# Optimization experiments

Hardware: AMD Instinct MI355X
Metric: run time of the kernel (lower is better)

Reference implementation:

```python
import jax, jax.numpy as jnp
import numpy as np

B, C, M, K, V, D, H, A, L, HF = 2, 128, 4, 4, 64, 1024, 16, 64, 4, 2048
E = M + K
EPS = 1e-5
THETA = 10000.0


def _rmsnorm(x, w):
    return x * jax.lax.rsqrt(jnp.mean(x * x, -1, keepdims=True) + EPS) * w


def _l2norm(x):
    n = jnp.sqrt(jnp.sum(x * x, -1, keepdims=True))
    return x / jnp.maximum(n, EPS)


def _rope(x, cos, sin):
    x1, x2 = jnp.split(x, 2, axis=-1)
    return jnp.concatenate([x1 * cos + x2 * sin, -x1 * sin + x2 * cos], -1)


def _forward(x_input, dec_w1, dec_w2, pos_emb, Wqkv, Wo, Wup, Wdown, attn_norm_w, ffn_norm_w, doc):
    b = x_input.shape[0]
    c = x_input.shape[1] // M
    # decoder_w1 then 'b (c m) (k v) -> b c k (m v)', decoder_w2, pos emb
    x = jnp.einsum('bsd,od->bso', x_input, dec_w1)
    x = x.reshape(b, c, M, K, V).transpose(0, 1, 3, 2, 4).reshape(b, c, K, M * V)
    x = jnp.einsum('bcku,du->bckd', x, dec_w2) + pos_emb
    # decoder_include_original_token: prepend original m tokens per block
    x = jnp.concatenate([x_input.reshape(b, c, M, D), x], axis=2).reshape(b, c * E, D)
    s = c * E
    # mask_mod (decoder_global_original_attn): (causal & kv%e<k & same_doc) | same_block
    idx = jnp.arange(s)
    blk = idx // E
    docs = doc[:, blk]  # [b, s]
    doc_m = docs[:, :, None] == docs[:, None, :]
    causal = blk[:, None] >= blk[None, :]
    kv_ok = (idx % E) < K
    same = blk[:, None] == blk[None, :]
    mask = (causal[None] & kv_ok[None, None, :] & doc_m) | same[None]  # [b, s, s]
    # rotary tables (applied post head-split, dim A)
    inv_freq = (1.0 / THETA) ** (jnp.arange(0, A, 2) / A)
    freqs = jnp.arange(s)[:, None] * inv_freq[None, :]
    cos, sin = jnp.cos(freqs), jnp.sin(freqs)  # [s, A/2]
    scale = 1.0 / jnp.sqrt(jnp.float32(A))
    neg = jnp.float32(-1e30)

    def heads(t):
        return t.reshape(b, s, H, A).transpose(0, 2, 1, 3)

    for li in range(L):
        xn = _rmsnorm(x, attn_norm_w[li])
        qkv = jnp.einsum('bsd,od->bso', xn, Wqkv[li])
        q, k, v = jnp.split(qkv, 3, axis=-1)
        q, k, v = heads(q), heads(k), heads(v)
        q, k = _l2norm(q), _l2norm(k)  # qk_norm
        q, k = _rope(q, cos, sin), _rope(k, cos, sin)
        scores = jnp.einsum('bhqa,bhka->bhqk', q, k) * scale
        scores = jnp.where(mask[:, None], scores, neg)
        probs = jax.nn.softmax(scores, axis=-1)
        attn = jnp.einsum('bhqk,bhka->bhqa', probs, v)
        attn = attn.transpose(0, 2, 1, 3).reshape(b, s, D)
        x1_in = jnp.einsum('bsd,od->bso', attn, Wo[li]) + x
        xf = _rmsnorm(x1_in, ffn_norm_w[li])
        up = jnp.einsum('bsd,od->bso', xf, Wup[li])
        u1, u2 = jnp.split(up, 2, axis=-1)
        x = jnp.einsum('bsh,dh->bsd', jax.nn.silu(u1) * u2, Wdown[li]) + x1_in
    # 'b (c e) d -> (b c) e d' then drop original tokens
    return x.reshape(b * c, E, D)[:, M:]


def setup_inputs() -> dict:
    key = jax.random.key(0)
    ks = jax.random.split(key, 10)
    sc = 0.02
    return {
        'x_input': jax.random.normal(ks[0], (B, C * M, D), jnp.float32),
        'doc': jnp.sort(jax.random.randint(ks[1], (B, C), 0, 4), axis=-1),
        'dec_w1': jax.random.normal(ks[2], (K * V, D), jnp.float32) * sc,
        'dec_w2': jax.random.normal(ks[3], (D, M * V), jnp.float32) * sc,
        'pos_emb': jax.random.normal(ks[4], (1, 1, K, D), jnp.float32) * sc,
        'Wqkv': jax.random.normal(ks[5], (L, 3 * D, D), jnp.float32) * sc,
        'Wo': jax.random.normal(ks[6], (L, D, D), jnp.float32) * sc,
        'Wup': jax.random.normal(ks[7], (L, 2 * HF, D), jnp.float32) * sc,
        'Wdown': jax.random.normal(ks[8], (L, D, HF), jnp.float32) * sc,
        'attn_norm_w': jnp.ones((L, D), jnp.float32),
        'ffn_norm_w': jnp.ones((L, D), jnp.float32),
    }


def reference(x_input, doc, dec_w1, dec_w2, pos_emb, Wqkv, Wo, Wup, Wdown, attn_norm_w, ffn_norm_w):
    return _forward(x_input, dec_w1, dec_w2, pos_emb, Wqkv, Wo, Wup, Wdown, attn_norm_w, ffn_norm_w, doc)
```

## Files before the change

kernel.cpp:

```cpp
#include <hip/hip_runtime.h>
#include <hip/hip_bf16.h>

typedef __bf16 bf16;
typedef __bf16 bf16x8 __attribute__((ext_vector_type(8)));
typedef __bf16 bf16x4 __attribute__((ext_vector_type(4)));
typedef float  f32x4  __attribute__((ext_vector_type(4)));

#define MFMA16(a, b, c) __builtin_amdgcn_mfma_f32_16x16x32_bf16(a, b, c, 0, 0, 0)

template <int EPI, int AF32, int BF32, int TM, int TN, int SK = 1>
__global__ __launch_bounds__(256 * SK) void gemm_bt(
    const void* __restrict__ Av, const void* __restrict__ Bv,
    const float* __restrict__ Res, void* __restrict__ Out,
    int Ntot, int Ktot, int lda)
{
    constexpr int PA = TM / 64, PB = TN / 64;
    constexpr int WN = (TN == 128) ? ((TM == 128) ? 2 : 4) : 2;
    constexpr int WM = 4 / WN;
    constexpr int I = TM / (WM * 16), J = TN / (WN * 16);
    __shared__ __align__(16) bf16 As[2][SK][TM][40];
    __shared__ __align__(16) bf16 Bs[2][SK][TN][40];
    static_assert(SK == 1 || sizeof(As) >= TM * TN * 4, "combine buffer fits in As");
    const int tid  = threadIdx.x;
    const int grp  = (SK > 1) ? (tid >> 8) : 0;
    const int t8   = tid & 255;
    const int wave = t8 >> 6, lane = tid & 63;
    const int quad = lane >> 4, l16 = lane & 15;
    const int wm = wave / WN, wn = wave % WN;
    const int rowW = wm * (TM / WM), colW = wn * (TN / WN);
    const int rowBase = blockIdx.y * TM, colBase = blockIdx.x * TN;

    f32x4 acc[I][J];
    const f32x4 z4 = {0.f, 0.f, 0.f, 0.f};
#pragma unroll
    for (int i = 0; i < I; i++)
#pragma unroll
        for (int j = 0; j < J; j++) acc[i][j] = z4;

    float4 rAf[PA][2]; bf16x8 rAb[PA];
    float4 rBf[PB][2]; bf16x8 rBb[PB];

    auto loadTile = [&](int kt) {
#pragma unroll
        for (int p = 0; p < PA; p++) {
            int ch = p * 256 + t8, r = ch >> 2, c8 = (ch & 3) << 3;
            if (AF32) {
                const float* s = (const float*)Av + (size_t)(rowBase + r) * lda + kt + c8;
                rAf[p][0] = *(const float4*)s; rAf[p][1] = *(const float4*)(s + 4);
            } else {
                rAb[p] = *(const bf16x8*)((const bf16*)Av + (size_t)(rowBase + r) * lda + kt + c8);
            }
        }
#pragma unroll
        for (int p = 0; p < PB; p++) {
            int ch = p * 256 + t8, r = ch >> 2, c8 = (ch & 3) << 3;
            if (BF32) {
                const float* s = (const float*)Bv + (size_t)(colBase + r) * Ktot + kt + c8;
                rBf[p][0] = *(const float4*)s; rBf[p][1] = *(const float4*)(s + 4);
            } else {
                rBb[p] = *(const bf16x8*)((const bf16*)Bv + (size_t)(colBase + r) * Ktot + kt + c8);
            }
        }
    };
    auto storeTile = [&](int buf) {
#pragma unroll
        for (int p = 0; p < PA; p++) {
            int ch = p * 256 + t8, r = ch >> 2, c8 = (ch & 3) << 3;
            bf16x8 t;
            if (AF32) {
                t[0]=(bf16)rAf[p][0].x; t[1]=(bf16)rAf[p][0].y; t[2]=(bf16)rAf[p][0].z; t[3]=(bf16)rAf[p][0].w;
                t[4]=(bf16)rAf[p][1].x; t[5]=(bf16)rAf[p][1].y; t[6]=(bf16)rAf[p][1].z; t[7]=(bf16)rAf[p][1].w;
            } else t = rAb[p];
            *(bf16x8*)&As[buf][grp][r][c8] = t;
        }
#pragma unroll
        for (int p = 0; p < PB; p++) {
            int ch = p * 256 + t8, r = ch >> 2, c8 = (ch & 3) << 3;
            bf16x8 t;
            if (BF32) {
                t[0]=(bf16)rBf[p][0].x; t[1]=(bf16)rBf[p][0].y; t[2]=(bf16)rBf[p][0].z; t[3]=(bf16)rBf[p][0].w;
                t[4]=(bf16)rBf[p][1].x; t[5]=(bf16)rBf[p][1].y; t[6]=(bf16)rBf[p][1].z; t[7]=(bf16)rBf[p][1].w;
            } else t = rBb[p];
            *(bf16x8*)&Bs[buf][grp][r][c8] = t;
        }
    };

    const int Kgrp  = Ktot / SK;
    const int kbase = grp * Kgrp;
    loadTile(kbase);
    storeTile(0);
    __syncthreads();
    const int nk = Kgrp >> 5;
    for (int k = 0; k < nk; k++) {
        const bool more = (k + 1) < nk;
        if (more) loadTile(kbase + ((k + 1) << 5));
        const int buf = k & 1;
        bf16x8 af[I], bfr[J];
#pragma unroll
        for (int i = 0; i < I; i++)
            af[i] = *(const bf16x8*)&As[buf][grp][rowW + i * 16 + l16][quad * 8];
#pragma unroll
        for (int j = 0; j < J; j++)
            bfr[j] = *(const bf16x8*)&Bs[buf][grp][colW + j * 16 + l16][quad * 8];
#pragma unroll
        for (int i = 0; i < I; i++)
#pragma unroll
            for (int j = 0; j < J; j++)
                acc[i][j] = MFMA16(af[i], bfr[j], acc[i][j]);
        if (more) { storeTile(buf ^ 1); __syncthreads(); }
    }

    if (SK == 2) {
        __syncthreads();
        float* red = (float*)&As[0][0][0][0];
        if (grp == 1) {
#pragma unroll
            for (int i = 0; i < I; i++)
#pragma unroll
                for (int j = 0; j < J; j++)
#pragma unroll
                    for (int r = 0; r < 4; r++)
                        red[(rowW + i * 16 + quad * 4 + r) * TN +
                            (colW + j * 16 + l16)] = acc[i][j][r];
        }
        __syncthreads();
        if (grp != 0) return;
#pragma unroll
        for (int i = 0; i < I; i++)
#pragma unroll
            for (int j = 0; j < J; j++)
#pragma unroll
                for (int r = 0; r < 4; r++)
                    acc[i][j][r] += red[(rowW + i * 16 + quad * 4 + r) * TN +
                                        (colW + j * 16 + l16)];
    }

#pragma unroll
    for (int i = 0; i < I; i++) {
        int row0 = rowBase + rowW + i * 16 + quad * 4;
#pragma unroll
        for (int j = 0; j < J; j++) {
            int col = colBase + colW + j * 16 + l16;
#pragma unroll
            for (int r = 0; r < 4; r++) {
                size_t off = (size_t)(row0 + r) * Ntot + col;
                float v = acc[i][j][r];
                if (EPI == 0)      ((bf16*)Out)[off]  = (bf16)v;
                else if (EPI == 1) ((float*)Out)[off] = v + Res[off];
                else               ((float*)Out)[off] = v;
            }
        }
    }
}

__global__ __launch_bounds__(512) void gemm_up_swiglu(
    const bf16* __restrict__ A, const float* __restrict__ B,
    bf16* __restrict__ Out)
{
    __shared__ __align__(16) bf16 Smem[2][2][256][40];
    const int tid  = threadIdx.x;
    const int grp  = tid >> 8, t8 = tid & 255;
    const int wave = t8 >> 6, lane = tid & 63;
    const int quad = lane >> 4, l16 = lane & 15;
    const int wm = wave >> 1, wn = wave & 1;
    const int rowBase = blockIdx.y * 128, cb = blockIdx.x;

    f32x4 acc[4][4];
    const f32x4 z4 = {0.f, 0.f, 0.f, 0.f};
#pragma unroll
    for (int i = 0; i < 4; i++)
#pragma unroll
        for (int j = 0; j < 4; j++) acc[i][j] = z4;

    bf16x8 rA[2]; float4 rB[2][2];
    auto loadTile = [&](int kt) {
#pragma unroll
        for (int p = 0; p < 2; p++) {
            int ch = p * 256 + t8, r = ch >> 2, c8 = (ch & 3) << 3;
            rA[p] = *(const bf16x8*)(A + (size_t)(rowBase + r) * 1024 + kt + c8);
            int brow = (r >> 6) * 2048 + cb * 64 + (r & 63);
            const float* s = B + (size_t)brow * 1024 + kt + c8;
            rB[p][0] = *(const float4*)s; rB[p][1] = *(const float4*)(s + 4);
        }
    };
    auto storeTile = [&](int buf) {
#pragma unroll
        for (int p = 0; p < 2; p++) {
            int ch = p * 256 + t8, r = ch >> 2, c8 = (ch & 3) << 3;
            *(bf16x8*)&Smem[buf][grp][r][c8] = rA[p];
            bf16x8 t;
            t[0]=(bf16)rB[p][0].x; t[1]=(bf16)rB[p][0].y; t[2]=(bf16)rB[p][0].z; t[3]=(bf16)rB[p][0].w;
            t[4]=(bf16)rB[p][1].x; t[5]=(bf16)rB[p][1].y; t[6]=(bf16)rB[p][1].z; t[7]=(bf16)rB[p][1].w;
            *(bf16x8*)&Smem[buf][grp][128 + r][c8] = t;
        }
    };

    const int kbase = grp * 512;
    loadTile(kbase);
    storeTile(0);
    __syncthreads();
    for (int k = 0; k < 16; k++) {
        const bool more = k < 15;
        if (more) loadTile(kbase + ((k + 1) << 5));
        const int buf = k & 1;
        bf16x8 af[4], bfr[4];
#pragma unroll
        for (int i = 0; i < 4; i++)
            af[i] = *(const bf16x8*)&Smem[buf][grp][wm * 64 + i * 16 + l16][quad * 8];
#pragma unroll
        for (int j = 0; j < 4; j++) {
            int brow = (j < 2) ? (wn * 32 + j * 16) : (64 + wn * 32 + (j - 2) * 16);
            bfr[j] = *(const bf16x8*)&Smem[buf][grp][128 + brow + l16][quad * 8];
        }
#pragma unroll
        for (int i = 0; i < 4; i++)
#pragma unroll
            for (int j = 0; j < 4; j++)
                acc[i][j] = MFMA16(af[i], bfr[j], acc[i][j]);
        if (more) { storeTile(buf ^ 1); __syncthreads(); }
    }

    __syncthreads();
    float* red = (float*)&Smem[0][0][0][0];
    if (grp == 1) {
#pragma unroll
        for (int i = 0; i < 4; i++)
#pragma unroll
            for (int j = 0; j < 4; j++) {
                int brow = ((j < 2) ? (wn * 32 + j * 16)
                                    : (64 + wn * 32 + (j - 2) * 16)) + l16;
#pragma unroll
                for (int r = 0; r < 4; r++)
                    red[(wm * 64 + i * 16 + quad * 4 + r) * 128 + brow] = acc[i][j][r];
            }
    }
    __syncthreads();
    if (grp != 0) return;
#pragma unroll
    for (int i = 0; i < 4; i++)
#pragma unroll
        for (int j = 0; j < 4; j++) {
            int brow = ((j < 2) ? (wn * 32 + j * 16)
                                : (64 + wn * 32 + (j - 2) * 16)) + l16;
#pragma unroll
            for (int r = 0; r < 4; r++)
                acc[i][j][r] += red[(wm * 64 + i * 16 + quad * 4 + r) * 128 + brow];
        }

#pragma unroll
    for (int i = 0; i < 4; i++) {
        int row0 = rowBase + wm * 64 + i * 16 + quad * 4;
#pragma unroll
        for (int jj = 0; jj < 2; jj++) {
            int col = cb * 64 + wn * 32 + jj * 16 + l16;
#pragma unroll
            for (int r = 0; r < 4; r++) {
                float u1 = acc[i][jj][r], u2 = acc[i][jj + 2][r];
                float g = u1 / (1.f + __expf(-u1));
                Out[(size_t)(row0 + r) * 2048 + col] = (bf16)(g * u2);
            }
        }
    }
}

__global__ __launch_bounds__(256) void rmsnorm_k(
    const float* __restrict__ X, const float* __restrict__ W,
    bf16* __restrict__ Out)
{
    const int row = blockIdx.x, tid = threadIdx.x;
    const float4 xv = *(const float4*)(X + (size_t)row * 1024 + tid * 4);
    float ss = xv.x * xv.x + xv.y * xv.y + xv.z * xv.z + xv.w * xv.w;
#pragma unroll
    for (int m = 1; m < 64; m <<= 1) ss += __shfl_xor(ss, m);
    __shared__ float red[4];
    if ((tid & 63) == 0) red[tid >> 6] = ss;
    __syncthreads();
    float tot = red[0] + red[1] + red[2] + red[3];
    float sc = rsqrtf(tot * (1.0f / 1024.0f) + 1e-5f);
    const float4 wv = *(const float4*)(W + tid * 4);
    bf16x4 o;
    o[0] = (bf16)(xv.x * sc * wv.x);
    o[1] = (bf16)(xv.y * sc * wv.y);
    o[2] = (bf16)(xv.z * sc * wv.z);
    o[3] = (bf16)(xv.w * sc * wv.w);
    *(bf16x4*)(Out + (size_t)row * 1024 + tid * 4) = o;
}

__global__ __launch_bounds__(256) void ropetab_k(float* __restrict__ tab)
{
    int i = blockIdx.x * 256 + threadIdx.x;
    int s = i >> 5, j = i & 31;
    float f = (float)s * __expf(-(float)j * 0.2878231366242557f);
    tab[i * 2]     = cosf(f);
    tab[i * 2 + 1] = sinf(f);
}

__global__ __launch_bounds__(256) void qkprep_k(
    bf16* __restrict__ qkv, const float* __restrict__ tab)
{
    int wid  = blockIdx.x * 4 + (threadIdx.x >> 6);
    int lane = threadIdx.x & 63;
    int s = wid & 1023, h = (wid >> 10) & 15, b = (wid >> 14) & 1, op = wid >> 15;
    bf16* addr = qkv + ((size_t)(b * 1024 + s)) * 3072 + op * 1024 + h * 64 + lane;
    float v = (float)*addr;
    float ss = v * v;
#pragma unroll
    for (int m = 1; m < 64; m <<= 1) ss += __shfl_xor(ss, m);
    v /= fmaxf(sqrtf(ss), 1e-5f);
    float2 cssn = ((const float2*)tab)[(s << 5) + (lane & 31)];
    float partner = __shfl_xor(v, 32);
    float o = (lane < 32) ? (v * cssn.x + partner * cssn.y)
                          : (v * cssn.x - partner * cssn.y);
    if (op == 0) o *= 0.125f;
    *addr = (bf16)o;
}

__global__ __launch_bounds__(256) void vtrans_k(
    const bf16* __restrict__ qkv, bf16* __restrict__ Vt,
    float* __restrict__ Oacc, float* __restrict__ lacc)
{
    __shared__ __align__(16) bf16 Ls[64][72];
    const int st = blockIdx.x, h = blockIdx.y, b = blockIdx.z;
    const int tid = threadIdx.x;

    int gi = ((b * 16 + h) * 16 + st) * 256 + tid;
    float* Oz = Oacc + (size_t)gi * 16;
    const float4 zf = {0.f, 0.f, 0.f, 0.f};
    *(float4*)Oz = zf; *(float4*)(Oz + 4) = zf;
    *(float4*)(Oz + 8) = zf; *(float4*)(Oz + 12) = zf;
    if (gi < 32768) lacc[gi] = 0.f;

#pragma unroll
    for (int p = 0; p < 2; p++) {
        int s = p * 32 + (tid >> 3), a0 = (tid & 7) << 3;
        *(bf16x8*)&Ls[s][a0] = *(const bf16x8*)(
            qkv + ((size_t)(b * 1024 + st * 64 + s)) * 3072 + 2048 + h * 64 + a0);
    }
    __syncthreads();
#pragma unroll
    for (int p = 0; p < 2; p++) {
        int a = p * 32 + (tid >> 3), s0 = (tid & 7) << 3;
        bf16x8 v;
#pragma unroll
        for (int j = 0; j < 8; j++) v[j] = Ls[s0 + j][a];
        *(bf16x8*)(Vt + (((size_t)((b * 16 + h) * 64 + a)) << 10) + st * 64 + s0) = v;
    }
}

__global__ __launch_bounds__(256) void attn_part(
    const bf16* __restrict__ qkv, const bf16* __restrict__ Vt,
    const int* __restrict__ doc,
    float* __restrict__ Oacc, float* __restrict__ lacc)
{
    const int h = blockIdx.y, b = blockIdx.z;
    const int tid = threadIdx.x, w = tid >> 6, lane = tid & 63;
    const int quad = lane >> 4, l16 = lane & 15;

    __shared__ __align__(16) char smraw[47616];
    bf16 (*Ks)[64][72]  = (bf16(*)[64][72])(smraw);
    bf16 (*Vs)[64][72]  = (bf16(*)[64][72])(smraw + 18432);
    bf16 (*PsT)[64][20] = (bf16(*)[64][20])(smraw + 36864);
    int* docL           = (int*)(smraw + 47104);

    if (tid < 128) docL[tid] = doc[b * 128 + tid];

    int xr = blockIdx.x, p = 0, c = 0;
    for (;;) {
        int ch = (p >> 2) + 1;
        if (xr < ch) { c = xr; break; }
        xr -= ch; p++;
    }
    const int ck0 = c * 4;
    const int T   = p + 1;
    const int ck1 = (ck0 + 4 < T) ? (ck0 + 4) : T;

    const int g = 4 * p + w;
    const bf16* qp = qkv + ((size_t)(b * 1024 + g * 16 + l16)) * 3072 + h * 64 + quad * 8;
    const bf16x8 qf0 = *(const bf16x8*)qp;
    const bf16x8 qf1 = *(const bf16x8*)(qp + 32);
    const bf16* Kbase = qkv + ((size_t)(b * 1024)) * 3072 + 1024 + h * 64;
    const bf16* Vbase = Vt + (((size_t)((b * 16 + h) * 64)) << 10);

    const f32x4 z4 = {0.f, 0.f, 0.f, 0.f};
    f32x4 O[4] = {z4, z4, z4, z4};
    float lp[4] = {0.f, 0.f, 0.f, 0.f};

    __syncthreads();
    int bq[4], dq[4];
#pragma unroll
    for (int r = 0; r < 4; r++) {
        bq[r] = (g * 16 + quad * 4 + r) >> 3;
        dq[r] = docL[bq[r]];
    }

    bf16x8 rK[2], rV[2];
    auto stageRegs = [&](int kt) {
#pragma unroll
        for (int cc = 0; cc < 2; cc++) {
            int ch = cc * 256 + tid, r = ch >> 3, c8 = (ch & 7) << 3;
            rK[cc] = *(const bf16x8*)(Kbase + (size_t)(kt * 64 + r) * 3072 + c8);
            rV[cc] = *(const bf16x8*)(Vbase + ((size_t)r << 10) + kt * 64 + c8);
        }
    };
    auto stageLDS = [&](int buf) {
#pragma unroll
        for (int cc = 0; cc < 2; cc++) {
            int ch = cc * 256 + tid, r = ch >> 3, c8 = (ch & 7) << 3;
            *(bf16x8*)&Ks[buf][r][c8] = rK[cc];
            *(bf16x8*)&Vs[buf][r][c8] = rV[cc];
        }
    };

    stageRegs(ck0);
    stageLDS(0);
    __syncthreads();
    for (int kt = ck0; kt < ck1; kt++) {
        const bool more = (kt + 1) < ck1;
        if (more) stageRegs(kt + 1);
        const int buf = (kt - ck0) & 1;
        const int k0 = kt * 64;
        f32x4 sf[4];
#pragma unroll
        for (int kg = 0; kg < 4; kg++) {
            const bf16x8 k0f = *(const bf16x8*)&Ks[buf][kg * 16 + l16][quad * 8];
            const bf16x8 k1f = *(const bf16x8*)&Ks[buf][kg * 16 + l16][32 + quad * 8];
            sf[kg] = z4;
            sf[kg] = MFMA16(qf0, k0f, sf[kg]);
            sf[kg] = MFMA16(qf1, k1f, sf[kg]);
        }
        float pvv[4][4];
#pragma unroll
        for (int kg = 0; kg < 4; kg++) {
            int kgi = k0 + kg * 16 + l16;
            int bk  = kgi >> 3;
            int dkv = docL[bk];
            bool kbit = (kgi & 7) < 4;
#pragma unroll
            for (int r = 0; r < 4; r++) {
                bool ok = (bq[r] == bk) || ((bq[r] >= bk) && kbit && (dq[r] == dkv));
                float pp = ok ? __expf(sf[kg][r]) : 0.f;
                pvv[kg][r] = pp;
                lp[r] += pp;
            }
        }
#pragma unroll
        for (int kg = 0; kg < 4; kg++) {
            bf16x4 t4;
#pragma unroll
            for (int r = 0; r < 4; r++) t4[r] = (bf16)pvv[kg][r];
            *(bf16x4*)&PsT[w][kg * 16 + l16][quad * 4] = t4;
        }
        bf16x8 pa0, pa1;
#pragma unroll
        for (int j = 0; j < 8; j++) {
            pa0[j] = PsT[w][quad * 8 + j][l16];
            pa1[j] = PsT[w][32 + quad * 8 + j][l16];
        }
#pragma unroll
        for (int t = 0; t < 4; t++) {
            const bf16x8 v0f = *(const bf16x8*)&Vs[buf][t * 16 + l16][quad * 8];
            const bf16x8 v1f = *(const bf16x8*)&Vs[buf][t * 16 + l16][32 + quad * 8];
            O[t] = MFMA16(pa0, v0f, O[t]);
            O[t] = MFMA16(pa1, v1f, O[t]);
        }
        if (more) stageLDS(buf ^ 1);
        __syncthreads();
    }

    float* Osc = (float*)smraw + w * 1024;
#pragma unroll
    for (int t = 0; t < 4; t++)
#pragma unroll
        for (int r = 0; r < 4; r++)
            Osc[(quad * 4 + r) * 64 + t * 16 + l16] = O[t][r];

#pragma unroll
    for (int r = 0; r < 4; r++) {
#pragma unroll
        for (int m = 1; m < 16; m <<= 1) lp[r] += __shfl_xor(lp[r], m);
    }
    const size_t rowb = (size_t)(b * 1024 + g * 16);
    if (l16 < 4) {
        float myl = (l16 == 0) ? lp[0] : (l16 == 1) ? lp[1] : (l16 == 2) ? lp[2] : lp[3];
        atomicAdd(&lacc[(rowb + quad * 4 + l16) * 16 + h], myl);
    }

    float* Obase = Oacc + rowb * 1024 + h * 64;
#pragma unroll
    for (int i = 0; i < 16; i++)
        atomicAdd(&Obase[(size_t)i * 1024 + lane], Osc[i * 64 + lane]);
}

__global__ __launch_bounds__(256) void attn_norm(
    const float* __restrict__ Oacc, const float* __restrict__ lacc,
    bf16* __restrict__ attnb)
{
    int i8 = (blockIdx.x * 256 + threadIdx.x) * 8;
    int row = i8 >> 10, d0 = i8 & 1023;
    float inv = 1.0f / fmaxf(lacc[row * 16 + (d0 >> 6)], 1e-20f);
    const float4 a = *(const float4*)(Oacc + i8);
    const float4 bvv = *(const float4*)(Oacc + i8 + 4);
    bf16x8 o;
    o[0] = (bf16)(a.x * inv); o[1] = (bf16)(a.y * inv);
    o[2] = (bf16)(a.z * inv); o[3] = (bf16)(a.w * inv);
    o[4] = (bf16)(bvv.x * inv); o[5] = (bf16)(bvv.y * inv);
    o[6] = (bf16)(bvv.z * inv); o[7] = (bf16)(bvv.w * inv);
    *(bf16x8*)(attnb + i8) = o;
}

__global__ __launch_bounds__(256) void permute_k(
    const bf16* __restrict__ t1, bf16* __restrict__ t1p)
{
    int idx = blockIdx.x * 256 + threadIdx.x;
    int u = idx & 255, m = u >> 6, v = u & 63;
    int orow = idx >> 8;
    int k = orow & 3, bc = orow >> 2;
    int b = bc >> 7, c = bc & 127;
    t1p[idx] = t1[((size_t)(b * 512 + c * 4 + m)) * 256 + k * 64 + v];
}

__global__ __launch_bounds__(256) void buildx_k(
    const float* __restrict__ x_input, const float* __restrict__ t2,
    const float* __restrict__ pos_emb, float* __restrict__ xres)
{
    int idx = blockIdx.x * 256 + threadIdx.x;
    int d = idx & 1023, row = idx >> 10;
    int b = row >> 10, rr = row & 1023;
    int c = rr >> 3, e = rr & 7;
    float v;
    if (e < 4)
        v = x_input[((size_t)(b * 512 + c * 4 + e)) * 1024 + d];
    else
        v = t2[((size_t)(b * 512 + c * 4 + (e - 4))) * 1024 + d] +
            pos_emb[(e - 4) * 1024 + d];
    xres[idx] = v;
}

__global__ __launch_bounds__(256) void finalout_k(
    const float* __restrict__ xres, float* __restrict__ out)
{
    int idx = blockIdx.x * 256 + threadIdx.x;
    int d = idx & 1023, t = idx >> 10;
    int kk = t & 3, bc = t >> 2;
    int b = bc >> 7, c = bc & 127;
    out[idx] = xres[((size_t)(b * 1024 + c * 8 + 4 + kk)) * 1024 + d];
}

extern "C" void kernel_launch(void* const* d_in, const int* in_sizes, int n_in,
                              void* d_out, int out_size, void* d_ws, size_t ws_size,
                              hipStream_t stream)
{
    const float* x_input = (const float*)d_in[0];
    const int*   doc     = (const int*)d_in[1];
    const float* dec_w1  = (const float*)d_in[2];
    const float* dec_w2  = (const float*)d_in[3];
    const float* pos_emb = (const float*)d_in[4];
    const float* Wqkv    = (const float*)d_in[5];
    const float* Wo      = (const float*)d_in[6];
    const float* Wup     = (const float*)d_in[7];
    const float* Wdown   = (const float*)d_in[8];
    const float* anw     = (const float*)d_in[9];
    const float* fnw     = (const float*)d_in[10];
    float* out = (float*)d_out;

    char* w = (char*)d_ws;
    float* xres  = (float*)(w);
    bf16*  xn1   = (bf16*)(w + (8u << 20));
    bf16*  xn2   = (bf16*)(w + (8u << 20));
    float* Oacc  = (float*)(w + (8u << 20));
    bf16*  t1    = (bf16*)(w + (8u << 20));
    bf16*  t1p   = (bf16*)(w + (8u << 20) + (512u << 10));
    bf16*  qkv   = (bf16*)(w + (16u << 20));
    float* t2    = (float*)(w + (16u << 20));
    float* x1res = (float*)(w + (16u << 20));
    bf16*  attnb = (bf16*)(w + (24u << 20));
    bf16*  hg    = (bf16*)(w + (24u << 20));
    bf16*  Vt    = (bf16*)(w + (28u << 20));
    float* rtab  = out;
    float* lacc  = out + 131072;

    ropetab_k<<<128, 256, 0, stream>>>(rtab);
    gemm_bt<0, 1, 1, 64, 64><<<dim3(4, 16), 256, 0, stream>>>(
        x_input, dec_w1, nullptr, t1, 256, 1024, 1024);
    permute_k<<<1024, 256, 0, stream>>>(t1, t1p);
    gemm_bt<2, 0, 1, 64, 64><<<dim3(16, 16), 256, 0, stream>>>(
        t1p, dec_w2, nullptr, t2, 1024, 256, 256);
    buildx_k<<<8192, 256, 0, stream>>>(x_input, t2, pos_emb, xres);

    for (int li = 0; li < 4; ++li) {
        rmsnorm_k<<<2048, 256, 0, stream>>>(xres, anw + li * 1024, xn1);
        gemm_bt<0, 0, 1, 128, 128><<<dim3(24, 16), 256, 0, stream>>>(
            xn1, Wqkv + (size_t)li * 3072 * 1024, nullptr, qkv, 3072, 1024, 1024);
        qkprep_k<<<16384, 256, 0, stream>>>(qkv, rtab);
        vtrans_k<<<dim3(16, 16, 2), 256, 0, stream>>>(qkv, Vt, Oacc, lacc);
        attn_part<<<dim3(40, 16, 2), 256, 0, stream>>>(qkv, Vt, doc, Oacc, lacc);
        attn_norm<<<1024, 256, 0, stream>>>(Oacc, lacc, attnb);
        gemm_bt<1, 0, 1, 64, 64, 2><<<dim3(16, 32), 512, 0, stream>>>(
            attnb, Wo + (size_t)li * 1024 * 1024, xres, x1res, 1024, 1024, 1024);
        rmsnorm_k<<<2048, 256, 0, stream>>>(x1res, fnw + li * 1024, xn2);
        gemm_up_swiglu<<<dim3(32, 16), 512, 0, stream>>>(
            xn2, Wup + (size_t)li * 4096 * 1024, hg);
        gemm_bt<1, 0, 1, 64, 64, 2><<<dim3(16, 32), 512, 0, stream>>>(
            hg, Wdown + (size_t)li * 1024 * 2048, x1res, xres, 1024, 2048, 2048);
    }

    finalout_k<<<4096, 256, 0, stream>>>(xres, out);
}
```

Baseline: 898.8 us.

## Fuse attention normalization into Wo GEMM, merge prep kernels, retile QKV and up GEMMs

The attention-normalization kernel is removed. The Wo GEMM now reads the fp32 Oacc directly and scales each row-head chunk by 1/l during the bf16 conversion. The qk-prep and V-transpose kernels are merged into one launch. The QKV GEMM moves from 128x128 tiles to 64x64 tiles with a split-K of 2, which gives more blocks. The SwiGLU up GEMM drops its split-K reduction and runs the full K loop with 256 threads. Residuals are updated in place in xres and the workspace layout is reshuffled, which saves launches and memory traffic but doubles A-load bandwidth for the Wo GEMM and risks aliasing bugs.

After: 914.1 us. About the same (+1.7%).

```diff
diff --git a/kernel.cpp b/kernel.cpp
--- a/kernel.cpp
+++ b/kernel.cpp
@@ -11,8 +11,8 @@
 template <int EPI, int AF32, int BF32, int TM, int TN, int SK = 1>
 __global__ __launch_bounds__(256 * SK) void gemm_bt(
     const void* __restrict__ Av, const void* __restrict__ Bv,
-    const float* __restrict__ Res, void* __restrict__ Out,
-    int Ntot, int Ktot, int lda)
+    const float* Res, void* Out,
+    int Ntot, int Ktot, int lda, const float* __restrict__ Lsc = nullptr)
 {
     constexpr int PA = TM / 64, PB = TN / 64;
     constexpr int WN = (TN == 128) ? ((TM == 128) ? 2 : 4) : 2;
@@ -37,7 +37,7 @@
 #pragma unroll
         for (int j = 0; j < J; j++) acc[i][j] = z4;
 
-    float4 rAf[PA][2]; bf16x8 rAb[PA];
+    float4 rAf[PA][2]; bf16x8 rAb[PA]; float linv[PA];
     float4 rBf[PB][2]; bf16x8 rBb[PB];
 
     auto loadTile = [&](int kt) {
@@ -47,6 +47,8 @@
             if (AF32) {
                 const float* s = (const float*)Av + (size_t)(rowBase + r) * lda + kt + c8;
                 rAf[p][0] = *(const float4*)s; rAf[p][1] = *(const float4*)(s + 4);
+                if (AF32 == 2)
+                    linv[p] = Lsc[(size_t)(rowBase + r) * 16 + (kt >> 6)];
             } else {
                 rAb[p] = *(const bf16x8*)((const bf16*)Av + (size_t)(rowBase + r) * lda + kt + c8);
             }
@@ -68,8 +70,11 @@
             int ch = p * 256 + t8, r = ch >> 2, c8 = (ch & 3) << 3;
             bf16x8 t;
             if (AF32) {
-                t[0]=(bf16)rAf[p][0].x; t[1]=(bf16)rAf[p][0].y; t[2]=(bf16)rAf[p][0].z; t[3]=(bf16)rAf[p][0].w;
-                t[4]=(bf16)rAf[p][1].x; t[5]=(bf16)rAf[p][1].y; t[6]=(bf16)rAf[p][1].z; t[7]=(bf16)rAf[p][1].w;
+                float sc = (AF32 == 2) ? (1.0f / fmaxf(linv[p], 1e-20f)) : 1.0f;
+                t[0]=(bf16)(rAf[p][0].x*sc); t[1]=(bf16)(rAf[p][0].y*sc);
+                t[2]=(bf16)(rAf[p][0].z*sc); t[3]=(bf16)(rAf[p][0].w*sc);
+                t[4]=(bf16)(rAf[p][1].x*sc); t[5]=(bf16)(rAf[p][1].y*sc);
+                t[6]=(bf16)(rAf[p][1].z*sc); t[7]=(bf16)(rAf[p][1].w*sc);
             } else t = rAb[p];
             *(bf16x8*)&As[buf][grp][r][c8] = t;
         }
@@ -153,14 +158,14 @@
     }
 }
 
-__global__ __launch_bounds__(512) void gemm_up_swiglu(
+__global__ __launch_bounds__(256) void gemm_up_swiglu(
     const bf16* __restrict__ A, const float* __restrict__ B,
     bf16* __restrict__ Out)
 {
-    __shared__ __align__(16) bf16 Smem[2][2][256][40];
+    __shared__ __align__(16) bf16 As[2][128][40];
+    __shared__ __align__(16) bf16 Bs[2][128][40];
     const int tid  = threadIdx.x;
-    const int grp  = tid >> 8, t8 = tid & 255;
-    const int wave = t8 >> 6, lane = tid & 63;
+    const int wave = tid >> 6, lane = tid & 63;
     const int quad = lane >> 4, l16 = lane & 15;
     const int wm = wave >> 1, wn = wave & 1;
     const int rowBase = blockIdx.y * 128, cb = blockIdx.x;
@@ -176,7 +181,7 @@
     auto loadTile = [&](int kt) {
 #pragma unroll
         for (int p = 0; p < 2; p++) {
-            int ch = p * 256 + t8, r = ch >> 2, c8 = (ch & 3) << 3;
+            int ch = p * 256 + tid, r = ch >> 2, c8 = (ch & 3) << 3;
             rA[p] = *(const bf16x8*)(A + (size_t)(rowBase + r) * 1024 + kt + c8);
             int brow = (r >> 6) * 2048 + cb * 64 + (r & 63);
             const float* s = B + (size_t)brow * 1024 + kt + c8;
@@ -186,31 +191,30 @@
     auto storeTile = [&](int buf) {
 #pragma unroll
         for (int p = 0; p < 2; p++) {
-            int ch = p * 256 + t8, r = ch >> 2, c8 = (ch & 3) << 3;
-            *(bf16x8*)&Smem[buf][grp][r][c8] = rA[p];
+            int ch = p * 256 + tid, r = ch >> 2, c8 = (ch & 3) << 3;
+            *(bf16x8*)&As[buf][r][c8] = rA[p];
             bf16x8 t;
             t[0]=(bf16)rB[p][0].x; t[1]=(bf16)rB[p][0].y; t[2]=(bf16)rB[p][0].z; t[3]=(bf16)rB[p][0].w;
             t[4]=(bf16)rB[p][1].x; t[5]=(bf16)rB[p][1].y; t[6]=(bf16)rB[p][1].z; t[7]=(bf16)rB[p][1].w;
-            *(bf16x8*)&Smem[buf][grp][128 + r][c8] = t;
+            *(bf16x8*)&Bs[buf][r][c8] = t;
         }
     };
 
-    const int kbase = grp * 512;
-    loadTile(kbase);
+    loadTile(0);
     storeTile(0);
     __syncthreads();
-    for (int k = 0; k < 16; k++) {
-        const bool more = k < 15;
-        if (more) loadTile(kbase + ((k + 1) << 5));
+    for (int k = 0; k < 32; k++) {
+        const bool more = k < 31;
+        if (more) loadTile((k + 1) << 5);
         const int buf = k & 1;
         bf16x8 af[4], bfr[4];
 #pragma unroll
         for (int i = 0; i < 4; i++)
-            af[i] = *(const bf16x8*)&Smem[buf][grp][wm * 64 + i * 16 + l16][quad * 8];
+            af[i] = *(const bf16x8*)&As[buf][wm * 64 + i * 16 + l16][quad * 8];
 #pragma unroll
         for (int j = 0; j < 4; j++) {
             int brow = (j < 2) ? (wn * 32 + j * 16) : (64 + wn * 32 + (j - 2) * 16);
-            bfr[j] = *(const bf16x8*)&Smem[buf][grp][128 + brow + l16][quad * 8];
+            bfr[j] = *(const bf16x8*)&Bs[buf][brow + l16][quad * 8];
         }
 #pragma unroll
         for (int i = 0; i < 4; i++)
@@ -219,33 +223,6 @@
                 acc[i][j] = MFMA16(af[i], bfr[j], acc[i][j]);
         if (more) { storeTile(buf ^ 1); __syncthreads(); }
     }
-
-    __syncthreads();
-    float* red = (float*)&Smem[0][0][0][0];
-    if (grp == 1) {
-#pragma unroll
-        for (int i = 0; i < 4; i++)
-#pragma unroll
-            for (int j = 0; j < 4; j++) {
-                int brow = ((j < 2) ? (wn * 32 + j * 16)
-                                    : (64 + wn * 32 + (j - 2) * 16)) + l16;
-#pragma unroll
-                for (int r = 0; r < 4; r++)
-                    red[(wm * 64 + i * 16 + quad * 4 + r) * 128 + brow] = acc[i][j][r];
-            }
-    }
-    __syncthreads();
-    if (grp != 0) return;
-#pragma unroll
-    for (int i = 0; i < 4; i++)
-#pragma unroll
-        for (int j = 0; j < 4; j++) {
-            int brow = ((j < 2) ? (wn * 32 + j * 16)
-                                : (64 + wn * 32 + (j - 2) * 16)) + l16;
-#pragma unroll
-            for (int r = 0; r < 4; r++)
-                acc[i][j][r] += red[(wm * 64 + i * 16 + quad * 4 + r) * 128 + brow];
-        }
 
 #pragma unroll
     for (int i = 0; i < 4; i++) {
@@ -295,55 +272,54 @@
     tab[i * 2 + 1] = sinf(f);
 }
 
-__global__ __launch_bounds__(256) void qkprep_k(
-    bf16* __restrict__ qkv, const float* __restrict__ tab)
-{
-    int wid  = blockIdx.x * 4 + (threadIdx.x >> 6);
-    int lane = threadIdx.x & 63;
-    int s = wid & 1023, h = (wid >> 10) & 15, b = (wid >> 14) & 1, op = wid >> 15;
-    bf16* addr = qkv + ((size_t)(b * 1024 + s)) * 3072 + op * 1024 + h * 64 + lane;
-    float v = (float)*addr;
-    float ss = v * v;
-#pragma unroll
-    for (int m = 1; m < 64; m <<= 1) ss += __shfl_xor(ss, m);
-    v /= fmaxf(sqrtf(ss), 1e-5f);
-    float2 cssn = ((const float2*)tab)[(s << 5) + (lane & 31)];
-    float partner = __shfl_xor(v, 32);
-    float o = (lane < 32) ? (v * cssn.x + partner * cssn.y)
-                          : (v * cssn.x - partner * cssn.y);
-    if (op == 0) o *= 0.125f;
-    *addr = (bf16)o;
-}
-
-__global__ __launch_bounds__(256) void vtrans_k(
-    const bf16* __restrict__ qkv, bf16* __restrict__ Vt,
-    float* __restrict__ Oacc, float* __restrict__ lacc)
+__global__ __launch_bounds__(256) void qkvprep_k(
+    bf16* __restrict__ qkv, const float* __restrict__ tab,
+    bf16* __restrict__ Vt, float* __restrict__ Oacc, float* __restrict__ lacc)
 {
     __shared__ __align__(16) bf16 Ls[64][72];
-    const int st = blockIdx.x, h = blockIdx.y, b = blockIdx.z;
     const int tid = threadIdx.x;
-
-    int gi = ((b * 16 + h) * 16 + st) * 256 + tid;
-    float* Oz = Oacc + (size_t)gi * 16;
-    const float4 zf = {0.f, 0.f, 0.f, 0.f};
-    *(float4*)Oz = zf; *(float4*)(Oz + 4) = zf;
-    *(float4*)(Oz + 8) = zf; *(float4*)(Oz + 12) = zf;
-    if (gi < 32768) lacc[gi] = 0.f;
-
-#pragma unroll
-    for (int p = 0; p < 2; p++) {
-        int s = p * 32 + (tid >> 3), a0 = (tid & 7) << 3;
-        *(bf16x8*)&Ls[s][a0] = *(const bf16x8*)(
-            qkv + ((size_t)(b * 1024 + st * 64 + s)) * 3072 + 2048 + h * 64 + a0);
-    }
-    __syncthreads();
-#pragma unroll
-    for (int p = 0; p < 2; p++) {
-        int a = p * 32 + (tid >> 3), s0 = (tid & 7) << 3;
-        bf16x8 v;
-#pragma unroll
-        for (int j = 0; j < 8; j++) v[j] = Ls[s0 + j][a];
-        *(bf16x8*)(Vt + (((size_t)((b * 16 + h) * 64 + a)) << 10) + st * 64 + s0) = v;
+    if (blockIdx.x < 16384) {
+        int wid  = blockIdx.x * 4 + (tid >> 6);
+        int lane = tid & 63;
+        int s = wid & 1023, h = (wid >> 10) & 15, b = (wid >> 14) & 1, op = wid >> 15;
+        bf16* addr = qkv + ((size_t)(b * 1024 + s)) * 3072 + op * 1024 + h * 64 + lane;
+        float v = (float)*addr;
+        float ss = v * v;
+#pragma unroll
+        for (int m = 1; m < 64; m <<= 1) ss += __shfl_xor(ss, m);
+        v /= fmaxf(sqrtf(ss), 1e-5f);
+        float2 cssn = ((const float2*)tab)[(s << 5) + (lane & 31)];
+        float partner = __shfl_xor(v, 32);
+        float o = (lane < 32) ? (v * cssn.x + partner * cssn.y)
+                              : (v * cssn.x - partner * cssn.y);
+        if (op == 0) o *= 0.125f;
+        *addr = (bf16)o;
+    } else {
+        int id = blockIdx.x - 16384;
+        int st = id & 15, h = (id >> 4) & 15, b = id >> 8;
+
+        int gi = ((b * 16 + h) * 16 + st) * 256 + tid;
+        float* Oz = Oacc + (size_t)gi * 16;
+        const float4 zf = {0.f, 0.f, 0.f, 0.f};
+        *(float4*)Oz = zf; *(float4*)(Oz + 4) = zf;
+        *(float4*)(Oz + 8) = zf; *(float4*)(Oz + 12) = zf;
+        if (gi < 32768) lacc[gi] = 0.f;
+
+#pragma unroll
+        for (int p = 0; p < 2; p++) {
+            int s = p * 32 + (tid >> 3), a0 = (tid & 7) << 3;
+            *(bf16x8*)&Ls[s][a0] = *(const bf16x8*)(
+                qkv + ((size_t)(b * 1024 + st * 64 + s)) * 3072 + 2048 + h * 64 + a0);
+        }
+        __syncthreads();
+#pragma unroll
+        for (int p = 0; p < 2; p++) {
+            int a = p * 32 + (tid >> 3), s0 = (tid & 7) << 3;
+            bf16x8 v;
+#pragma unroll
+            for (int j = 0; j < 8; j++) v[j] = Ls[s0 + j][a];
+            *(bf16x8*)(Vt + (((size_t)((b * 16 + h) * 64 + a)) << 10) + st * 64 + s0) = v;
+        }
     }
 }
 
@@ -484,28 +460,10 @@
         float myl = (l16 == 0) ? lp[0] : (l16 == 1) ? lp[1] : (l16 == 2) ? lp[2] : lp[3];
         atomicAdd(&lacc[(rowb + quad * 4 + l16) * 16 + h], myl);
     }
-
     float* Obase = Oacc + rowb * 1024 + h * 64;
 #pragma unroll
     for (int i = 0; i < 16; i++)
         atomicAdd(&Obase[(size_t)i * 1024 + lane], Osc[i * 64 + lane]);
-}
-
-__global__ __launch_bounds__(256) void attn_norm(
-    const float* __restrict__ Oacc, const float* __restrict__ lacc,
-    bf16* __restrict__ attnb)
-{
-    int i8 = (blockIdx.x * 256 + threadIdx.x) * 8;
-    int row = i8 >> 10, d0 = i8 & 1023;
-    float inv = 1.0f / fmaxf(lacc[row * 16 + (d0 >> 6)], 1e-20f);
-    const float4 a = *(const float4*)(Oacc + i8);
-    const float4 bvv = *(const float4*)(Oacc + i8 + 4);
-    bf16x8 o;
-    o[0] = (bf16)(a.x * inv); o[1] = (bf16)(a.y * inv);
-    o[2] = (bf16)(a.z * inv); o[3] = (bf16)(a.w * inv);
-    o[4] = (bf16)(bvv.x * inv); o[5] = (bf16)(bvv.y * inv);
-    o[6] = (bf16)(bvv.z * inv); o[7] = (bf16)(bvv.w * inv);
-    *(bf16x8*)(attnb + i8) = o;
 }
 
 __global__ __launch_bounds__(256) void permute_k(
@@ -565,17 +523,15 @@
 
     char* w = (char*)d_ws;
     float* xres  = (float*)(w);
-    bf16*  xn1   = (bf16*)(w + (8u << 20));
-    bf16*  xn2   = (bf16*)(w + (8u << 20));
     float* Oacc  = (float*)(w + (8u << 20));
     bf16*  t1    = (bf16*)(w + (8u << 20));
     bf16*  t1p   = (bf16*)(w + (8u << 20) + (512u << 10));
-    bf16*  qkv   = (bf16*)(w + (16u << 20));
+    bf16*  xn1   = (bf16*)(w + (16u << 20));
+    bf16*  Vt    = (bf16*)(w + (16u << 20));
+    bf16*  xn2   = (bf16*)(w + (16u << 20));
     float* t2    = (float*)(w + (16u << 20));
-    float* x1res = (float*)(w + (16u << 20));
-    bf16*  attnb = (bf16*)(w + (24u << 20));
+    bf16*  qkv   = (bf16*)(w + (20u << 20));
     bf16*  hg    = (bf16*)(w + (24u << 20));
-    bf16*  Vt    = (bf16*)(w + (28u << 20));
     float* rtab  = out;
     float* lacc  = out + 131072;
 
@@ -589,19 +545,17 @@
 
     for (int li = 0; li < 4; ++li) {
         rmsnorm_k<<<2048, 256, 0, stream>>>(xres, anw + li * 1024, xn1);
-        gemm_bt<0, 0, 1, 128, 128><<<dim3(24, 16), 256, 0, stream>>>(
+        gemm_bt<0, 0, 1, 64, 64, 2><<<dim3(48, 32), 512, 0, stream>>>(
             xn1, Wqkv + (size_t)li * 3072 * 1024, nullptr, qkv, 3072, 1024, 1024);
-        qkprep_k<<<16384, 256, 0, stream>>>(qkv, rtab);
-        vtrans_k<<<dim3(16, 16, 2), 256, 0, stream>>>(qkv, Vt, Oacc, lacc);
+        qkvprep_k<<<16896, 256, 0, stream>>>(qkv, rtab, Vt, Oacc, lacc);
         attn_part<<<dim3(40, 16, 2), 256, 0, stream>>>(qkv, Vt, doc, Oacc, lacc);
-        attn_norm<<<1024, 256, 0, stream>>>(Oacc, lacc, attnb);
-        gemm_bt<1, 0, 1, 64, 64, 2><<<dim3(16, 32), 512, 0, stream>>>(
-            attnb, Wo + (size_t)li * 1024 * 1024, xres, x1res, 1024, 1024, 1024);
-        rmsnorm_k<<<2048, 256, 0, stream>>>(x1res, fnw + li * 1024, xn2);
-        gemm_up_swiglu<<<dim3(32, 16), 512, 0, stream>>>(
+        gemm_bt<1, 2, 1, 64, 64, 2><<<dim3(16, 32), 512, 0, stream>>>(
+            Oacc, Wo + (size_t)li * 1024 * 1024, xres, xres, 1024, 1024, 1024, lacc);
+        rmsnorm_k<<<2048, 256, 0, stream>>>(xres, fnw + li * 1024, xn2);
+        gemm_up_swiglu<<<dim3(32, 16), 256, 0, stream>>>(
             xn2, Wup + (size_t)li * 4096 * 1024, hg);
         gemm_bt<1, 0, 1, 64, 64, 2><<<dim3(16, 32), 512, 0, stream>>>(
-            hg, Wdown + (size_t)li * 1024 * 2048, x1res, xres, 1024, 2048, 2048);
+            hg, Wdown + (size_t)li * 1024 * 2048, xres, xres, 1024, 2048, 2048);
     }
 
     finalout_k<<<4096, 256, 0, stream>>>(xres, out);
```
